# Kernel optimization log

Hardware: AMD Instinct MI355X
Metric: run time of the kernel (lower is better)

## Reference

```python
import jax, jax.numpy as jnp
import numpy as np

NCTX, RANK, DIM = 32, 64, 8192
ID = 65536
DD_PER = ID // NCTX  # 2048 intrinsic dims per context token
LL = 8192            # next power of two >= DIM (here equal to DIM)


def setup_inputs() -> dict:
    key = jax.random.key(0)
    ks = jax.random.split(key, 8)
    U = jax.random.normal(ks[0], (NCTX, RANK), dtype=jnp.float32)
    s = jax.random.normal(ks[1], (RANK,), dtype=jnp.float32)
    V = jax.random.normal(ks[2], (DD_PER, RANK), dtype=jnp.float32)
    shared_V = jax.random.normal(ks[3], (DD_PER,), dtype=jnp.float32)
    initial = jax.random.normal(ks[4], (NCTX, DIM), dtype=jnp.float32)
    # Rademacher +/-1 diagonal per context token
    BB = jnp.where(jax.random.normal(ks[5], (NCTX, LL)) >= 0, 1.0, -1.0).astype(jnp.float32)
    GG = jax.random.normal(ks[6], (NCTX, LL), dtype=jnp.float32)
    # independent permutation of [0, LL) per context token
    Pi = jnp.argsort(jax.random.uniform(ks[7], (NCTX, LL)), axis=1).astype(jnp.int32)
    return {"U": U, "s": s, "V": V, "shared_V": shared_V,
            "initial": initial, "BB": BB, "GG": GG, "Pi": Pi}


def wht(x):
    """Unnormalized fast Walsh-Hadamard transform over last axis. x: (B, L), L pow2."""
    B, L = x.shape
    h = 1
    while h < L:
        xr = x.reshape(B, L // (2 * h), 2, h)
        a, b = xr[:, :, 0, :], xr[:, :, 1, :]
        x = jnp.stack((a + b, a - b), axis=2).reshape(B, L)
        h *= 2
    return x


def fastfood(x, BB, Pi, GG):
    """Batched fastfood projection: x (nctx, dd) -> (nctx, DIM)."""
    nctx, dd = x.shape
    xp = jnp.pad(x, ((0, 0), (0, LL - dd)))          # pad to LL
    m = wht(xp * BB)                                  # H B x
    m = jnp.take_along_axis(m, Pi, axis=1) * GG       # G Pi H B x
    m = wht(m)                                        # H G Pi H B x
    divisor = jnp.sqrt(LL * jnp.sum(GG * GG, axis=1, keepdims=True))
    return m[:, :DIM] / (divisor * np.sqrt(float(DIM) / LL))


def reference(U, s, V, shared_V, initial, BB, GG, Pi):
    # low-rank reconstruction: (nctx, DD_PER)
    recon = jnp.einsum('lr,r,dr->ld', U, s, V) + shared_V[None, :]
    ray = fastfood(recon, BB, Pi, GG)                 # (nctx, DIM)
    return initial + ray
```

## Files before the change

kernel.cpp:

```cpp
#include <hip/hip_runtime.h>
#include <math.h>

#define NCTXC 32
#define RANKC 64
#define LLC   8192
#define DDC   2048
#define NT    256
#define NPROD 64
#define MAGIC 0x5CA1AB1Eu

__device__ __forceinline__ int swz(int j) { return j ^ (((j >> 5) & 7) << 2); }

__device__ __forceinline__ void bfly(float& a, float& b) {
    float p = a + b, q = a - b;
    a = p; b = q;
}
__device__ __forceinline__ void radix8(float* r) {
    bfly(r[0],r[1]); bfly(r[2],r[3]); bfly(r[4],r[5]); bfly(r[6],r[7]);
    bfly(r[0],r[2]); bfly(r[1],r[3]); bfly(r[4],r[6]); bfly(r[5],r[7]);
    bfly(r[0],r[4]); bfly(r[1],r[5]); bfly(r[2],r[6]); bfly(r[3],r[7]);
}
__device__ __forceinline__ void radix4(float& a, float& b, float& c, float& d) {
    bfly(a,b); bfly(c,d);
    bfly(a,c); bfly(b,d);
}
template<int N>
__device__ __forceinline__ void shfl_stages(float* r, int t) {
#pragma unroll
    for (int mi = 0; mi < 6; ++mi) {
        const int m = 1 << mi;
        const float sgn = (t & m) ? -1.f : 1.f;
#pragma unroll
        for (int k = 0; k < N; ++k) {
            float p = __shfl_xor(r[k], m);
            r[k] = fmaf(sgn, r[k], p);
        }
    }
}

__global__ __launch_bounds__(NT, 1) void intrinsic_fused_kernel(
    const float* __restrict__ U, const float* __restrict__ s,
    const float* __restrict__ V, const float* __restrict__ sharedV,
    const float* __restrict__ initial, const float* __restrict__ BB,
    const float* __restrict__ GG, const int* __restrict__ Pi,
    float* __restrict__ out, float* __restrict__ x0,
    unsigned int* __restrict__ flags)
{
    const int bid = blockIdx.x;
    const int t   = threadIdx.x;

    if (bid < NPROD) {
        const int d0 = bid * 32;
        const int l  = t >> 3;
        const int d  = d0 + 4 * (t & 7);

        const float4* U4 = (const float4*)U;
        const float4* s4 = (const float4*)s;
        const float4* V4 = (const float4*)V;

        float4 w4[16];
#pragma unroll
        for (int r4 = 0; r4 < 16; ++r4) {
            float4 u = U4[l * 16 + r4];
            float4 sv = s4[r4];
            w4[r4] = make_float4(u.x * sv.x, u.y * sv.y, u.z * sv.z, u.w * sv.w);
        }
        float acc[4];
#pragma unroll
        for (int c = 0; c < 4; ++c) {
            const float4* Vr = V4 + (size_t)(d + c) * 16;
            float a = 0.f;
#pragma unroll
            for (int r4 = 0; r4 < 16; ++r4) {
                float4 v = Vr[r4];
                a += w4[r4].x * v.x + w4[r4].y * v.y + w4[r4].z * v.z + w4[r4].w * v.w;
            }
            acc[c] = a;
        }
        float4 sh = *(const float4*)(sharedV + d);
        float4 bb = *(const float4*)(BB + (size_t)l * LLC + d);
        *(float4*)(x0 + (size_t)l * DDC + d) =
            make_float4((acc[0] + sh.x) * bb.x, (acc[1] + sh.y) * bb.y,
                        (acc[2] + sh.z) * bb.z, (acc[3] + sh.w) * bb.w);
        __syncthreads();
        if (t == 0)
            __hip_atomic_store(&flags[bid], MAGIC, __ATOMIC_RELEASE,
                               __HIP_MEMORY_SCOPE_AGENT);
        return;
    }

    __shared__ __align__(16) float xs[DDC];
    __shared__ __align__(16) float ys[LLC];
    __shared__ float wsum[4];

    const int l = bid - NPROD;

    const int4*   PiP = (const int4*)(Pi + (size_t)l * LLC);
    const float4* GGP = (const float4*)(GG + (size_t)l * LLC);
    const float2* InP = (const float2*)(initial + (size_t)l * LLC);
    int4 pi[4][2]; float4 gg[4][2]; float2 iv[4][4];
#pragma unroll
    for (int c = 0; c < 4; ++c) {
        pi[c][0] = PiP[2 * t + 512 * c];
        pi[c][1] = PiP[2 * t + 512 * c + 1];
        gg[c][0] = GGP[2 * t + 512 * c];
        gg[c][1] = GGP[2 * t + 512 * c + 1];
    }
#pragma unroll
    for (int c = 0; c < 4; ++c)
#pragma unroll
        for (int d = 0; d < 4; ++d)
            iv[c][d] = InP[t + 256 * d + 1024 * c];

    float gs = 0.f;
#pragma unroll
    for (int c = 0; c < 4; ++c)
#pragma unroll
        for (int h = 0; h < 2; ++h) {
            float4 g = gg[c][h];
            gs += g.x * g.x + g.y * g.y + g.z * g.z + g.w * g.w;
        }
#pragma unroll
    for (int off = 32; off > 0; off >>= 1) gs += __shfl_down(gs, off);
    if ((t & 63) == 0) wsum[t >> 6] = gs;

    if (t < NPROD)
        while (__hip_atomic_load(&flags[t], __ATOMIC_ACQUIRE,
                                 __HIP_MEMORY_SCOPE_AGENT) != MAGIC) {}
    __syncthreads();

    float r[8];
    {
        const float4* xr = (const float4*)(x0 + (size_t)l * DDC);
        float4 a0 = xr[2 * t], a1 = xr[2 * t + 1];
        r[0]=a0.x; r[1]=a0.y; r[2]=a0.z; r[3]=a0.w;
        r[4]=a1.x; r[5]=a1.y; r[6]=a1.z; r[7]=a1.w;
        radix8(r);
        shfl_stages<8>(r, t);
        *(float4*)(xs + swz(8 * t))     = make_float4(r[0], r[1], r[2], r[3]);
        *(float4*)(xs + swz(8 * t + 4)) = make_float4(r[4], r[5], r[6], r[7]);
    }
    __syncthreads();
    {
        float2 g2[4];
#pragma unroll
        for (int d = 0; d < 4; ++d)
            g2[d] = *(const float2*)(xs + swz(2 * t + 512 * d));
        radix4(g2[0].x, g2[1].x, g2[2].x, g2[3].x);
        radix4(g2[0].y, g2[1].y, g2[2].y, g2[3].y);
#pragma unroll
        for (int d = 0; d < 4; ++d)
            *(float2*)(xs + swz(2 * t + 512 * d)) = g2[d];
    }
    __syncthreads();

    {
        float rb[4][8];
#pragma unroll
        for (int c = 0; c < 4; ++c) {
            int4 p0 = pi[c][0], p1 = pi[c][1];
            float4 g0 = gg[c][0], g1 = gg[c][1];
            rb[c][0] = xs[swz(p0.x & 2047)] * g0.x;
            rb[c][1] = xs[swz(p0.y & 2047)] * g0.y;
            rb[c][2] = xs[swz(p0.z & 2047)] * g0.z;
            rb[c][3] = xs[swz(p0.w & 2047)] * g0.w;
            rb[c][4] = xs[swz(p1.x & 2047)] * g1.x;
            rb[c][5] = xs[swz(p1.y & 2047)] * g1.y;
            rb[c][6] = xs[swz(p1.z & 2047)] * g1.z;
            rb[c][7] = xs[swz(p1.w & 2047)] * g1.w;
        }
#pragma unroll
        for (int c = 0; c < 4; ++c) radix8(rb[c]);
#pragma unroll
        for (int mi = 0; mi < 6; ++mi) {
            const int m = 1 << mi;
            const float sgn = (t & m) ? -1.f : 1.f;
#pragma unroll
            for (int c = 0; c < 4; ++c)
#pragma unroll
                for (int k = 0; k < 8; ++k) {
                    float p = __shfl_xor(rb[c][k], m);
                    rb[c][k] = fmaf(sgn, rb[c][k], p);
                }
        }
#pragma unroll
        for (int c = 0; c < 4; ++c) {
            *(float4*)(ys + swz(8 * t + 2048 * c)) =
                make_float4(rb[c][0], rb[c][1], rb[c][2], rb[c][3]);
            *(float4*)(ys + swz(8 * t + 4 + 2048 * c)) =
                make_float4(rb[c][4], rb[c][5], rb[c][6], rb[c][7]);
        }
    }
    __syncthreads();

    {
        float invd = rsqrtf(8192.f *
                            ((wsum[0] + wsum[1]) + (wsum[2] + wsum[3])));
        float2 q[4][4];
#pragma unroll
        for (int c = 0; c < 4; ++c)
#pragma unroll
            for (int d = 0; d < 4; ++d)
                q[c][d] = *(const float2*)(ys + swz(2 * t + 512 * d + 2048 * c));
#pragma unroll
        for (int c = 0; c < 4; ++c) {
            radix4(q[c][0].x, q[c][1].x, q[c][2].x, q[c][3].x);
            radix4(q[c][0].y, q[c][1].y, q[c][2].y, q[c][3].y);
        }
#pragma unroll
        for (int d = 0; d < 4; ++d) {
            radix4(q[0][d].x, q[1][d].x, q[2][d].x, q[3][d].x);
            radix4(q[0][d].y, q[1][d].y, q[2][d].y, q[3][d].y);
        }
        float2* OutP = (float2*)(out + (size_t)l * LLC);
#pragma unroll
        for (int c = 0; c < 4; ++c)
#pragma unroll
            for (int d = 0; d < 4; ++d) {
                float2 a = iv[c][d];
                OutP[t + 256 * d + 1024 * c] =
                    make_float2(a.x + q[c][d].x * invd, a.y + q[c][d].y * invd);
            }
    }
}

extern "C" void kernel_launch(void* const* d_in, const int* in_sizes, int n_in,
                              void* d_out, int out_size, void* d_ws, size_t ws_size,
                              hipStream_t stream) {
    const float* U       = (const float*)d_in[0];
    const float* s       = (const float*)d_in[1];
    const float* V       = (const float*)d_in[2];
    const float* sharedV = (const float*)d_in[3];
    const float* initial = (const float*)d_in[4];
    const float* BB      = (const float*)d_in[5];
    const float* GG      = (const float*)d_in[6];
    const int*   Pi      = (const int*)d_in[7];
    float* out = (float*)d_out;

    float*        x0    = (float*)d_ws;
    unsigned int* flags = (unsigned int*)((char*)d_ws + (1 << 20));

    intrinsic_fused_kernel<<<dim3(NPROD + NCTXC), dim3(NT), 0, stream>>>(
        U, s, V, sharedV, initial, BB, GG, Pi, out, x0, flags);
}
```

Measured before the change: 15.18 us.

## Restructure Walsh-Hadamard stages to cut shuffles and move butterflies into producers

Producer blocks now run the first 32-point butterfly stages (in-register radix-4 plus three xor-shuffle stages) before writing x0, so the consumer does less of the first transform. The second WHT stops using 6 shuffle stages over 32 values per thread. Each thread instead does a 32-point in-register transform on contiguous gathered elements, then two 16-point float4 passes through shared memory run by half the threads. The shared-memory swizzle is dropped, and the initial/output accesses are widened to float4 on 128 threads. This trades many cross-lane shuffles for more shared-memory round trips and idle threads, with possible bank conflicts now that there is no swizzle.

Result: slower. 15.48 us (+2.0%).

```diff
diff --git a/kernel.cpp b/kernel.cpp
--- a/kernel.cpp
+++ b/kernel.cpp
@@ -9,33 +9,12 @@
 #define NPROD 64
 #define MAGIC 0x5CA1AB1Eu
 
-__device__ __forceinline__ int swz(int j) { return j ^ (((j >> 5) & 7) << 2); }
-
 __device__ __forceinline__ void bfly(float& a, float& b) {
     float p = a + b, q = a - b;
     a = p; b = q;
 }
-__device__ __forceinline__ void radix8(float* r) {
-    bfly(r[0],r[1]); bfly(r[2],r[3]); bfly(r[4],r[5]); bfly(r[6],r[7]);
-    bfly(r[0],r[2]); bfly(r[1],r[3]); bfly(r[4],r[6]); bfly(r[5],r[7]);
-    bfly(r[0],r[4]); bfly(r[1],r[5]); bfly(r[2],r[6]); bfly(r[3],r[7]);
-}
-__device__ __forceinline__ void radix4(float& a, float& b, float& c, float& d) {
-    bfly(a,b); bfly(c,d);
-    bfly(a,c); bfly(b,d);
-}
-template<int N>
-__device__ __forceinline__ void shfl_stages(float* r, int t) {
-#pragma unroll
-    for (int mi = 0; mi < 6; ++mi) {
-        const int m = 1 << mi;
-        const float sgn = (t & m) ? -1.f : 1.f;
-#pragma unroll
-        for (int k = 0; k < N; ++k) {
-            float p = __shfl_xor(r[k], m);
-            r[k] = fmaf(sgn, r[k], p);
-        }
-    }
+__device__ __forceinline__ void bfly4(float4& a, float4& b) {
+    bfly(a.x, b.x); bfly(a.y, b.y); bfly(a.z, b.z); bfly(a.w, b.w);
 }
 
 __global__ __launch_bounds__(NT, 1) void intrinsic_fused_kernel(
@@ -52,7 +31,7 @@
     if (bid < NPROD) {
         const int d0 = bid * 32;
         const int l  = t >> 3;
-        const int d  = d0 + 4 * (t & 7);
+        const int i0 = 4 * (t & 7);
 
         const float4* U4 = (const float4*)U;
         const float4* s4 = (const float4*)s;
@@ -65,23 +44,39 @@
             float4 sv = s4[r4];
             w4[r4] = make_float4(u.x * sv.x, u.y * sv.y, u.z * sv.z, u.w * sv.w);
         }
-        float acc[4];
+        float v[4];
 #pragma unroll
         for (int c = 0; c < 4; ++c) {
-            const float4* Vr = V4 + (size_t)(d + c) * 16;
+            const float4* Vr = V4 + (size_t)(d0 + i0 + c) * 16;
             float a = 0.f;
 #pragma unroll
             for (int r4 = 0; r4 < 16; ++r4) {
-                float4 v = Vr[r4];
-                a += w4[r4].x * v.x + w4[r4].y * v.y + w4[r4].z * v.z + w4[r4].w * v.w;
+                float4 vv = Vr[r4];
+                a += w4[r4].x * vv.x + w4[r4].y * vv.y +
+                     w4[r4].z * vv.z + w4[r4].w * vv.w;
             }
-            acc[c] = a;
-        }
-        float4 sh = *(const float4*)(sharedV + d);
-        float4 bb = *(const float4*)(BB + (size_t)l * LLC + d);
-        *(float4*)(x0 + (size_t)l * DDC + d) =
-            make_float4((acc[0] + sh.x) * bb.x, (acc[1] + sh.y) * bb.y,
-                        (acc[2] + sh.z) * bb.z, (acc[3] + sh.w) * bb.w);
+            v[c] = a;
+        }
+        float4 sh = *(const float4*)(sharedV + d0 + i0);
+        float4 bb = *(const float4*)(BB + (size_t)l * LLC + d0 + i0);
+        v[0] = (v[0] + sh.x) * bb.x;  v[1] = (v[1] + sh.y) * bb.y;
+        v[2] = (v[2] + sh.z) * bb.z;  v[3] = (v[3] + sh.w) * bb.w;
+
+        bfly(v[0], v[1]); bfly(v[2], v[3]);
+        bfly(v[0], v[2]); bfly(v[1], v[3]);
+#pragma unroll
+        for (int mi = 0; mi < 3; ++mi) {
+            const int m = 1 << mi;
+            const float sgn = (t & m) ? -1.f : 1.f;
+#pragma unroll
+            for (int c = 0; c < 4; ++c) {
+                float p = __shfl_xor(v[c], m);
+                v[c] = fmaf(sgn, v[c], p);
+            }
+        }
+        *(float4*)(x0 + (size_t)l * DDC + d0 + i0) =
+            make_float4(v[0], v[1], v[2], v[3]);
+
         __syncthreads();
         if (t == 0)
             __hip_atomic_store(&flags[bid], MAGIC, __ATOMIC_RELEASE,
@@ -95,31 +90,25 @@
 
     const int l = bid - NPROD;
 
-    const int4*   PiP = (const int4*)(Pi + (size_t)l * LLC);
-    const float4* GGP = (const float4*)(GG + (size_t)l * LLC);
-    const float2* InP = (const float2*)(initial + (size_t)l * LLC);
-    int4 pi[4][2]; float4 gg[4][2]; float2 iv[4][4];
-#pragma unroll
-    for (int c = 0; c < 4; ++c) {
-        pi[c][0] = PiP[2 * t + 512 * c];
-        pi[c][1] = PiP[2 * t + 512 * c + 1];
-        gg[c][0] = GGP[2 * t + 512 * c];
-        gg[c][1] = GGP[2 * t + 512 * c + 1];
-    }
-#pragma unroll
-    for (int c = 0; c < 4; ++c)
-#pragma unroll
-        for (int d = 0; d < 4; ++d)
-            iv[c][d] = InP[t + 256 * d + 1024 * c];
+    const int4*   PiP = (const int4*)(Pi + (size_t)l * LLC) + 8 * t;
+    const float4* GGP = (const float4*)(GG + (size_t)l * LLC) + 8 * t;
+    int4 pi[8]; float4 gg[8];
+#pragma unroll
+    for (int u = 0; u < 8; ++u) { pi[u] = PiP[u]; gg[u] = GGP[u]; }
+
+    float4 iv[16];
+    if (t < 128) {
+        const float4* InP = (const float4*)(initial + (size_t)l * LLC);
+#pragma unroll
+        for (int m = 0; m < 16; ++m) iv[m] = InP[t + 128 * m];
+    }
 
     float gs = 0.f;
 #pragma unroll
-    for (int c = 0; c < 4; ++c)
-#pragma unroll
-        for (int h = 0; h < 2; ++h) {
-            float4 g = gg[c][h];
-            gs += g.x * g.x + g.y * g.y + g.z * g.z + g.w * g.w;
-        }
+    for (int u = 0; u < 8; ++u) {
+        float4 g = gg[u];
+        gs += g.x * g.x + g.y * g.y + g.z * g.z + g.w * g.w;
+    }
 #pragma unroll
     for (int off = 32; off > 0; off >>= 1) gs += __shfl_down(gs, off);
     if ((t & 63) == 0) wsum[t >> 6] = gs;
@@ -129,98 +118,101 @@
                                  __HIP_MEMORY_SCOPE_AGENT) != MAGIC) {}
     __syncthreads();
 
-    float r[8];
     {
-        const float4* xr = (const float4*)(x0 + (size_t)l * DDC);
-        float4 a0 = xr[2 * t], a1 = xr[2 * t + 1];
-        r[0]=a0.x; r[1]=a0.y; r[2]=a0.z; r[3]=a0.w;
-        r[4]=a1.x; r[5]=a1.y; r[6]=a1.z; r[7]=a1.w;
-        radix8(r);
-        shfl_stages<8>(r, t);
-        *(float4*)(xs + swz(8 * t))     = make_float4(r[0], r[1], r[2], r[3]);
-        *(float4*)(xs + swz(8 * t + 4)) = make_float4(r[4], r[5], r[6], r[7]);
-    }
-    __syncthreads();
+        const float* xrow = x0 + (size_t)l * DDC + (t & 31) + 256 * (t >> 5);
+        float r[8];
+#pragma unroll
+        for (int e = 0; e < 8; ++e) r[e] = xrow[32 * e];
+#pragma unroll
+        for (int h = 1; h < 8; h <<= 1)
+#pragma unroll
+            for (int k = 0; k < 8; ++k)
+                if (!(k & h)) bfly(r[k], r[k + h]);
+        const float sgn = (t & 32) ? -1.f : 1.f;
+#pragma unroll
+        for (int e = 0; e < 8; ++e) {
+            float p = __shfl_xor(r[e], 32);
+            r[e] = fmaf(sgn, r[e], p);
+        }
+        float* xw = xs + (t & 31) + 256 * (t >> 5);
+#pragma unroll
+        for (int e = 0; e < 8; ++e) xw[32 * e] = r[e];
+    }
+    __syncthreads();
+
     {
-        float2 g2[4];
-#pragma unroll
-        for (int d = 0; d < 4; ++d)
-            g2[d] = *(const float2*)(xs + swz(2 * t + 512 * d));
-        radix4(g2[0].x, g2[1].x, g2[2].x, g2[3].x);
-        radix4(g2[0].y, g2[1].y, g2[2].y, g2[3].y);
-#pragma unroll
-        for (int d = 0; d < 4; ++d)
-            *(float2*)(xs + swz(2 * t + 512 * d)) = g2[d];
+        float2* xs2 = (float2*)xs;
+        float2 g[4];
+#pragma unroll
+        for (int d = 0; d < 4; ++d) g[d] = xs2[t + 256 * d];
+        bfly(g[0].x, g[1].x); bfly(g[2].x, g[3].x);
+        bfly(g[0].y, g[1].y); bfly(g[2].y, g[3].y);
+        bfly(g[0].x, g[2].x); bfly(g[1].x, g[3].x);
+        bfly(g[0].y, g[2].y); bfly(g[1].y, g[3].y);
+#pragma unroll
+        for (int d = 0; d < 4; ++d) xs2[t + 256 * d] = g[d];
     }
     __syncthreads();
 
     {
-        float rb[4][8];
-#pragma unroll
-        for (int c = 0; c < 4; ++c) {
-            int4 p0 = pi[c][0], p1 = pi[c][1];
-            float4 g0 = gg[c][0], g1 = gg[c][1];
-            rb[c][0] = xs[swz(p0.x & 2047)] * g0.x;
-            rb[c][1] = xs[swz(p0.y & 2047)] * g0.y;
-            rb[c][2] = xs[swz(p0.z & 2047)] * g0.z;
-            rb[c][3] = xs[swz(p0.w & 2047)] * g0.w;
-            rb[c][4] = xs[swz(p1.x & 2047)] * g1.x;
-            rb[c][5] = xs[swz(p1.y & 2047)] * g1.y;
-            rb[c][6] = xs[swz(p1.z & 2047)] * g1.z;
-            rb[c][7] = xs[swz(p1.w & 2047)] * g1.w;
-        }
-#pragma unroll
-        for (int c = 0; c < 4; ++c) radix8(rb[c]);
-#pragma unroll
-        for (int mi = 0; mi < 6; ++mi) {
-            const int m = 1 << mi;
-            const float sgn = (t & m) ? -1.f : 1.f;
-#pragma unroll
-            for (int c = 0; c < 4; ++c)
-#pragma unroll
-                for (int k = 0; k < 8; ++k) {
-                    float p = __shfl_xor(rb[c][k], m);
-                    rb[c][k] = fmaf(sgn, rb[c][k], p);
-                }
-        }
-#pragma unroll
-        for (int c = 0; c < 4; ++c) {
-            *(float4*)(ys + swz(8 * t + 2048 * c)) =
-                make_float4(rb[c][0], rb[c][1], rb[c][2], rb[c][3]);
-            *(float4*)(ys + swz(8 * t + 4 + 2048 * c)) =
-                make_float4(rb[c][4], rb[c][5], rb[c][6], rb[c][7]);
-        }
-    }
-    __syncthreads();
-
-    {
-        float invd = rsqrtf(8192.f *
-                            ((wsum[0] + wsum[1]) + (wsum[2] + wsum[3])));
-        float2 q[4][4];
-#pragma unroll
-        for (int c = 0; c < 4; ++c)
-#pragma unroll
-            for (int d = 0; d < 4; ++d)
-                q[c][d] = *(const float2*)(ys + swz(2 * t + 512 * d + 2048 * c));
-#pragma unroll
-        for (int c = 0; c < 4; ++c) {
-            radix4(q[c][0].x, q[c][1].x, q[c][2].x, q[c][3].x);
-            radix4(q[c][0].y, q[c][1].y, q[c][2].y, q[c][3].y);
-        }
-#pragma unroll
-        for (int d = 0; d < 4; ++d) {
-            radix4(q[0][d].x, q[1][d].x, q[2][d].x, q[3][d].x);
-            radix4(q[0][d].y, q[1][d].y, q[2][d].y, q[3][d].y);
-        }
-        float2* OutP = (float2*)(out + (size_t)l * LLC);
-#pragma unroll
-        for (int c = 0; c < 4; ++c)
-#pragma unroll
-            for (int d = 0; d < 4; ++d) {
-                float2 a = iv[c][d];
-                OutP[t + 256 * d + 1024 * c] =
-                    make_float2(a.x + q[c][d].x * invd, a.y + q[c][d].y * invd);
-            }
+        float r[32];
+#pragma unroll
+        for (int u = 0; u < 8; ++u) {
+            int4 p = pi[u]; float4 g = gg[u];
+            r[4*u+0] = xs[p.x & 2047] * g.x;
+            r[4*u+1] = xs[p.y & 2047] * g.y;
+            r[4*u+2] = xs[p.z & 2047] * g.z;
+            r[4*u+3] = xs[p.w & 2047] * g.w;
+        }
+#pragma unroll
+        for (int h = 1; h < 32; h <<= 1)
+#pragma unroll
+            for (int k = 0; k < 32; ++k)
+                if (!(k & h)) bfly(r[k], r[k + h]);
+        float4* ys4 = (float4*)ys;
+#pragma unroll
+        for (int u = 0; u < 8; ++u)
+            ys4[8 * t + u] = make_float4(r[4*u], r[4*u+1], r[4*u+2], r[4*u+3]);
+    }
+    __syncthreads();
+
+    if (t < 128) {
+        float4* ys4 = (float4*)ys;
+        const int b2 = (t & 7) + 128 * (t >> 3);
+        float4 q[16];
+#pragma unroll
+        for (int n = 0; n < 16; ++n) q[n] = ys4[b2 + 8 * n];
+#pragma unroll
+        for (int h = 1; h < 16; h <<= 1)
+#pragma unroll
+            for (int k = 0; k < 16; ++k)
+                if (!(k & h)) bfly4(q[k], q[k + h]);
+#pragma unroll
+        for (int n = 0; n < 16; ++n) ys4[b2 + 8 * n] = q[n];
+    }
+    __syncthreads();
+
+    if (t < 128) {
+        float4* ys4 = (float4*)ys;
+        float4 q[16];
+#pragma unroll
+        for (int m = 0; m < 16; ++m) q[m] = ys4[t + 128 * m];
+#pragma unroll
+        for (int h = 1; h < 16; h <<= 1)
+#pragma unroll
+            for (int k = 0; k < 16; ++k)
+                if (!(k & h)) bfly4(q[k], q[k + h]);
+        const float invd =
+            rsqrtf(8192.f * ((wsum[0] + wsum[1]) + (wsum[2] + wsum[3])));
+        float4* OutP = (float4*)(out + (size_t)l * LLC);
+#pragma unroll
+        for (int m = 0; m < 16; ++m) {
+            float4 a = iv[m];
+            OutP[t + 128 * m] = make_float4(a.x + q[m].x * invd,
+                                            a.y + q[m].y * invd,
+                                            a.z + q[m].z * invd,
+                                            a.w + q[m].w * invd);
+        }
     }
 }
 
```
